# Optimization experiments

Measured on AMD Instinct MI355X. Metric: run time of the kernel, lower is better.

## Reference

```python
import jax, jax.numpy as jnp
import numpy as np

N_HEAD = 16
W = 128  # one-sided window = attention_window // 2


def setup_inputs() -> dict:
    key = jax.random.key(0)
    ks = jax.random.split(key, 6)
    B, S, D = 4, 1536, 1024
    init = lambda k: jax.random.normal(k, (D, D), jnp.float32) * 0.02
    return {
        "x": jax.random.normal(ks[0], (B, S, D), jnp.float32),
        "Wq": init(ks[1]), "bq": jnp.zeros((D,), jnp.float32),
        "Wk": init(ks[2]),
        "Wv": init(ks[3]), "bv": jnp.zeros((D,), jnp.float32),
        "Wo": init(ks[4]), "bo": jnp.zeros((D,), jnp.float32),
    }


def _local_attention(q, k, v, w):
    """Sliding-window attention. q,k,v: [B,H,S,Dh]; q,k pre-scaled.
    Returns context [B,H,S,Dh] and banded logits qk [B,S,H,2w+1] (fp32)."""
    B, H, S, Dh = q.shape
    C = S // w  # number of w-sized query chunks
    pad = [(0, 0), (0, 0), (w, w), (0, 0)]
    kp = jnp.pad(k, pad)
    vp = jnp.pad(v, pad)
    # key/value chunks: chunk c sees padded positions [c*w, c*w + 3w)
    idx = jnp.arange(C)[:, None] * w + jnp.arange(3 * w)[None, :]  # [C,3w]
    kc = kp[:, :, idx]                      # [B,H,C,3w,Dh]
    vc = vp[:, :, idx]                      # [B,H,C,3w,Dh]
    qc = q.reshape(B, H, C, w, Dh)          # [B,H,C,w,Dh]
    scores = jnp.einsum('bhcxd,bhcyd->bhcxy', qc, kc)  # [B,H,C,w,3w]
    # extract diagonal band: query x attends to chunk-local keys y = x .. x+2w
    xi = jnp.arange(w)[:, None]             # [w,1]
    jj = jnp.arange(2 * w + 1)[None, :]     # [1,2w+1]
    y = xi + jj                             # [w,2w+1], values in [0,3w)
    band = jnp.take_along_axis(scores, y[None, None, None], axis=-1)  # [B,H,C,w,2w+1]
    # mask positions whose absolute key index falls outside [0,S)
    key_pos = jnp.arange(C)[:, None, None] * w + xi[None] + jj[None] - w  # [C,w,2w+1]
    valid = (key_pos >= 0) & (key_pos < S)
    band = jnp.where(valid[None, None], band, -jnp.inf)
    prob = jax.nn.softmax(band.astype(jnp.float32), axis=-1).astype(q.dtype)
    # scatter band probs back to chunk layout, then contract with value chunks
    scat = jnp.zeros_like(scores).at[..., xi, y].set(prob)  # [B,H,C,w,3w]
    ctx = jnp.einsum('bhcxy,bhcyd->bhcxd', scat, vc).reshape(B, H, S, Dh)
    qk = band.astype(jnp.float32).reshape(B, H, S, 2 * w + 1).transpose(0, 2, 1, 3)
    return ctx, qk


def reference(x, Wq, bq, Wk, Wv, bv, Wo, bo):
    B, S, D = x.shape
    H, Dh = N_HEAD, D // N_HEAD
    scale = Dh ** (-0.25)
    q = ((x @ Wq.T + bq).reshape(B, S, H, Dh).transpose(0, 2, 1, 3)) * scale
    k = ((x @ Wk.T).reshape(B, S, H, Dh).transpose(0, 2, 1, 3)) * scale
    v = (x @ Wv.T + bv).reshape(B, S, H, Dh).transpose(0, 2, 1, 3)
    ctx, qk = _local_attention(q, k, v, W)
    wv = ctx.transpose(0, 2, 1, 3).reshape(B, S, D)
    out = wv @ Wo.T + bo
    return out, qk
```

## Files before the change

kernel.cpp:

```cpp
#include <hip/hip_runtime.h>

#define S_LEN  1536
#define NH     16
#define DHEAD  64
#define WIN    128
#define BAND   257
#define DMODEL 1024
#define BATCH  4
#define MROWS  (BATCH * S_LEN)

#define SQ    32
#define SWIN  (SQ + 2*WIN)
#define WKEYS 320
#define PST   296

#define NEG_BIG (-3.0e38f)

typedef __attribute__((ext_vector_type(8))) short frag_ab;
typedef __attribute__((ext_vector_type(4))) float frag_cd;
typedef __attribute__((ext_vector_type(8))) unsigned short ushort8v;

__device__ __forceinline__ unsigned short f2bf(float f) {
  unsigned u = __float_as_uint(f);
  u += 0x7FFFu + ((u >> 16) & 1u);
  return (unsigned short)(u >> 16);
}
__device__ __forceinline__ float bf2f(unsigned short h) {
  return __uint_as_float(((unsigned)h) << 16);
}

__device__ __forceinline__ void gload16(const unsigned short* g, unsigned short* l) {
  __builtin_amdgcn_global_load_lds(
      (const __attribute__((address_space(1))) unsigned int*)g,
      (__attribute__((address_space(3))) unsigned int*)l, 16, 0, 0);
}

__device__ __forceinline__ int swz4(int r) { return (r & 3) ^ ((r >> 2) & 3); }

__global__ __launch_bounds__(256)
void convert_hilo(const float* __restrict__ src, unsigned short* __restrict__ hi,
                  unsigned short* __restrict__ lo, int n4)
{
  const int i = blockIdx.x * 256 + threadIdx.x;
  if (i >= n4) return;
  const float4 v = reinterpret_cast<const float4*>(src)[i];
  unsigned short h0 = f2bf(v.x), h1 = f2bf(v.y), h2 = f2bf(v.z), h3 = f2bf(v.w);
  unsigned short l0 = f2bf(v.x - bf2f(h0)), l1 = f2bf(v.y - bf2f(h1));
  unsigned short l2 = f2bf(v.z - bf2f(h2)), l3 = f2bf(v.w - bf2f(h3));
  uint2 hp, lp;
  hp.x = (unsigned)h0 | ((unsigned)h1 << 16); hp.y = (unsigned)h2 | ((unsigned)h3 << 16);
  lp.x = (unsigned)l0 | ((unsigned)l1 << 16); lp.y = (unsigned)l2 | ((unsigned)l3 << 16);
  reinterpret_cast<uint2*>(hi)[i] = hp;
  reinterpret_cast<uint2*>(lo)[i] = lp;
}

__global__ __launch_bounds__(256)
void copy_f4(const float4* __restrict__ src, float4* __restrict__ dst, int n4)
{
  const int i = blockIdx.x * 256 + threadIdx.x;
  if (i < n4) dst[i] = src[i];
}

__global__ __launch_bounds__(256)
void mfma_gemm_qkv(const unsigned short* __restrict__ Ah_g,
                   const unsigned short* __restrict__ Al_g,
                   const unsigned short* __restrict__ Bh_g,
                   const unsigned short* __restrict__ Bl_g,
                   const float* __restrict__ bq, const float* __restrict__ bv,
                   float scale,
                   unsigned short* __restrict__ Qh, unsigned short* __restrict__ Ql,
                   unsigned short* __restrict__ Kh, unsigned short* __restrict__ Kl,
                   unsigned short* __restrict__ Vh, unsigned short* __restrict__ Vl)
{
  __shared__ __align__(16) unsigned short Ah[128*32];
  __shared__ __align__(16) unsigned short Al[128*32];
  __shared__ __align__(16) unsigned short Bh[128*32];
  __shared__ __align__(16) unsigned short Bl[128*32];

  const int t    = threadIdx.x;
  const int wave = t >> 6, lane = t & 63;
  const int wr   = wave >> 1, wc = wave & 1;

  const int bid  = blockIdx.x;
  const int xcd  = bid & 7;
  const int r    = bid >> 3;
  const int n0   = (xcd*3 + (r % 3)) * 128;
  const int m0   = (r / 3) * 128;

  frag_cd acc[4][4];
#pragma unroll
  for (int i = 0; i < 4; ++i)
#pragma unroll
    for (int j = 0; j < 4; ++j) acc[i][j] = (frag_cd){0.f,0.f,0.f,0.f};

  const int srow = lane >> 2;
  const int scol = ((lane & 3) ^ swz4(srow)) * 8;
  const unsigned short* pa0 = Ah_g + (size_t)(m0 + wave*32      + srow) * DMODEL + scol;
  const unsigned short* pa1 = Ah_g + (size_t)(m0 + wave*32 + 16 + srow) * DMODEL + scol;
  const unsigned short* qa0 = Al_g + (size_t)(m0 + wave*32      + srow) * DMODEL + scol;
  const unsigned short* qa1 = Al_g + (size_t)(m0 + wave*32 + 16 + srow) * DMODEL + scol;
  const unsigned short* pb0 = Bh_g + (size_t)(n0 + wave*32      + srow) * DMODEL + scol;
  const unsigned short* pb1 = Bh_g + (size_t)(n0 + wave*32 + 16 + srow) * DMODEL + scol;
  const unsigned short* qb0 = Bl_g + (size_t)(n0 + wave*32      + srow) * DMODEL + scol;
  const unsigned short* qb1 = Bl_g + (size_t)(n0 + wave*32 + 16 + srow) * DMODEL + scol;
  unsigned short* lA0 = &Ah[(wave*32)*32];
  unsigned short* lA1 = &Ah[(wave*32+16)*32];
  unsigned short* lL0 = &Al[(wave*32)*32];
  unsigned short* lL1 = &Al[(wave*32+16)*32];
  unsigned short* lB0 = &Bh[(wave*32)*32];
  unsigned short* lB1 = &Bh[(wave*32+16)*32];
  unsigned short* lC0 = &Bl[(wave*32)*32];
  unsigned short* lC1 = &Bl[(wave*32+16)*32];

  const int l16  = lane & 15;
  const int koff = ((lane >> 4) * 8) ^ (swz4(l16) * 8);
  int ofsA[4], ofsB[4];
#pragma unroll
  for (int i = 0; i < 4; ++i) ofsA[i] = (wr*64 + i*16 + l16)*32 + koff;
#pragma unroll
  for (int j = 0; j < 4; ++j) ofsB[j] = (wc*64 + j*16 + l16)*32 + koff;

  for (int k0 = 0; k0 < DMODEL; k0 += 32) {
    gload16(pa0, lA0); gload16(pa1, lA1);
    gload16(qa0, lL0); gload16(qa1, lL1);
    gload16(pb0, lB0); gload16(pb1, lB1);
    gload16(qb0, lC0); gload16(qb1, lC1);
    pa0 += 32; pa1 += 32; qa0 += 32; qa1 += 32;
    pb0 += 32; pb1 += 32; qb0 += 32; qb1 += 32;
    __syncthreads();

    frag_ab ah[4], alr[4];
#pragma unroll
    for (int i = 0; i < 4; ++i) {
      ah[i]  = *reinterpret_cast<const frag_ab*>(&Ah[ofsA[i]]);
      alr[i] = *reinterpret_cast<const frag_ab*>(&Al[ofsA[i]]);
    }
#pragma unroll
    for (int j = 0; j < 4; ++j) {
      frag_ab bh  = *reinterpret_cast<const frag_ab*>(&Bh[ofsB[j]]);
      frag_ab blr = *reinterpret_cast<const frag_ab*>(&Bl[ofsB[j]]);
#pragma unroll
      for (int i = 0; i < 4; ++i) {
        acc[i][j] = __builtin_amdgcn_mfma_f32_16x16x32_bf16(ah[i],  bh,  acc[i][j], 0,0,0);
        acc[i][j] = __builtin_amdgcn_mfma_f32_16x16x32_bf16(ah[i],  blr, acc[i][j], 0,0,0);
        acc[i][j] = __builtin_amdgcn_mfma_f32_16x16x32_bf16(alr[i], bh,  acc[i][j], 0,0,0);
      }
    }
    __syncthreads();
  }

  const int rg = lane >> 4;
  const int which = n0 >> 10;
  const float sc = (which < 2) ? scale : 1.0f;
  const float* bias = (which == 0) ? bq : ((which == 2) ? bv : nullptr);
  unsigned short* Dh = (which == 0) ? Qh : ((which == 1) ? Kh : Vh);
  unsigned short* Dl = (which == 0) ? Ql : ((which == 1) ? Kl : Vl);
#pragma unroll
  for (int j = 0; j < 4; ++j) {
    const int n  = n0 + wc*64 + j*16 + l16;
    const int nn = n & 1023;
    const float bval = bias ? bias[nn] : 0.f;
    const int hh = nn >> 6, dh = nn & 63;
#pragma unroll
    for (int i = 0; i < 4; ++i) {
#pragma unroll
      for (int r2 = 0; r2 < 4; ++r2) {
        const int m = m0 + wr*64 + i*16 + rg*4 + r2;
        const int b = m / S_LEN;
        const int s = m - b * S_LEN;
        const size_t idx = ((size_t)((b*NH + hh)*S_LEN + s))*DHEAD + dh;
        const float v = (acc[i][j][r2] + bval) * sc;
        const unsigned short hv = f2bf(v);
        Dh[idx] = hv;
        Dl[idx] = f2bf(v - bf2f(hv));
      }
    }
  }
}

__global__ __launch_bounds__(256)
void mfma_gemm_bt(const unsigned short* __restrict__ Ah_g,
                  const unsigned short* __restrict__ Al_g,
                  const unsigned short* __restrict__ Bh_g,
                  const unsigned short* __restrict__ Bl_g,
                  const float* __restrict__ bias, float scale,
                  float* __restrict__ Cf)
{
  __shared__ __align__(16) unsigned short Ah[128*32];
  __shared__ __align__(16) unsigned short Al[128*32];
  __shared__ __align__(16) unsigned short Bh[64*32];
  __shared__ __align__(16) unsigned short Bl[64*32];

  const int t    = threadIdx.x;
  const int wave = t >> 6, lane = t & 63;
  const int wr   = wave >> 1, wc = wave & 1;
  const int m0   = blockIdx.y * 128;
  const int n0   = blockIdx.x * 64;

  frag_cd acc[4][2];
#pragma unroll
  for (int i = 0; i < 4; ++i)
#pragma unroll
    for (int j = 0; j < 2; ++j) acc[i][j] = (frag_cd){0.f,0.f,0.f,0.f};

  const int srow = lane >> 2;
  const int scol = ((lane & 3) ^ swz4(srow)) * 8;
  const unsigned short* pa0 = Ah_g + (size_t)(m0 + wave*32      + srow) * DMODEL + scol;
  const unsigned short* pa1 = Ah_g + (size_t)(m0 + wave*32 + 16 + srow) * DMODEL + scol;
  const unsigned short* qa0 = Al_g + (size_t)(m0 + wave*32      + srow) * DMODEL + scol;
  const unsigned short* qa1 = Al_g + (size_t)(m0 + wave*32 + 16 + srow) * DMODEL + scol;
  const unsigned short* pb  = Bh_g + (size_t)(n0 + wave*16      + srow) * DMODEL + scol;
  const unsigned short* qb  = Bl_g + (size_t)(n0 + wave*16      + srow) * DMODEL + scol;
  unsigned short* lA0 = &Ah[(wave*32)*32];
  unsigned short* lA1 = &Ah[(wave*32+16)*32];
  unsigned short* lL0 = &Al[(wave*32)*32];
  unsigned short* lL1 = &Al[(wave*32+16)*32];
  unsigned short* lB  = &Bh[(wave*16)*32];
  unsigned short* lBl = &Bl[(wave*16)*32];

  const int l16  = lane & 15;
  const int koff = ((lane >> 4) * 8) ^ (swz4(l16) * 8);
  int ofsA[4], ofsB[2];
#pragma unroll
  for (int i = 0; i < 4; ++i) ofsA[i] = (wr*64 + i*16 + l16)*32 + koff;
#pragma unroll
  for (int j = 0; j < 2; ++j) ofsB[j] = (wc*32 + j*16 + l16)*32 + koff;

  for (int k0 = 0; k0 < DMODEL; k0 += 32) {
    gload16(pa0, lA0); gload16(pa1, lA1);
    gload16(qa0, lL0); gload16(qa1, lL1);
    gload16(pb,  lB);  gload16(qb,  lBl);
    pa0 += 32; pa1 += 32; qa0 += 32; qa1 += 32; pb += 32; qb += 32;
    __syncthreads();

    frag_ab ah[4], alr[4], bh[2], blr[2];
#pragma unroll
    for (int i = 0; i < 4; ++i) {
      ah[i]  = *reinterpret_cast<const frag_ab*>(&Ah[ofsA[i]]);
      alr[i] = *reinterpret_cast<const frag_ab*>(&Al[ofsA[i]]);
    }
#pragma unroll
    for (int j = 0; j < 2; ++j) {
      bh[j]  = *reinterpret_cast<const frag_ab*>(&Bh[ofsB[j]]);
      blr[j] = *reinterpret_cast<const frag_ab*>(&Bl[ofsB[j]]);
    }
#pragma unroll
    for (int i = 0; i < 4; ++i)
#pragma unroll
      for (int j = 0; j < 2; ++j) {
        acc[i][j] = __builtin_amdgcn_mfma_f32_16x16x32_bf16(ah[i],  bh[j],  acc[i][j], 0,0,0);
        acc[i][j] = __builtin_amdgcn_mfma_f32_16x16x32_bf16(ah[i],  blr[j], acc[i][j], 0,0,0);
        acc[i][j] = __builtin_amdgcn_mfma_f32_16x16x32_bf16(alr[i], bh[j],  acc[i][j], 0,0,0);
      }
    __syncthreads();
  }

  const int rg = lane >> 4;
#pragma unroll
  for (int j = 0; j < 2; ++j) {
    const int n = n0 + wc*32 + j*16 + l16;
    const float bval = bias ? bias[n] : 0.f;
#pragma unroll
    for (int i = 0; i < 4; ++i) {
#pragma unroll
      for (int r = 0; r < 4; ++r) {
        const int m = m0 + wr*64 + i*16 + rg*4 + r;
        Cf[(size_t)m * DMODEL + n] = (acc[i][j][r] + bval) * scale;
      }
    }
  }
}

__global__ __launch_bounds__(256, 3)
void attn_fused(const unsigned short* __restrict__ Qh_g, const unsigned short* __restrict__ Ql_g,
                const unsigned short* __restrict__ Kh_g, const unsigned short* __restrict__ Kl_g,
                const unsigned short* __restrict__ Vh_g, const unsigned short* __restrict__ Vl_g,
                float* __restrict__ qk,
                unsigned short* __restrict__ ctx_hi, unsigned short* __restrict__ ctx_lo)
{
  __shared__ __align__(16) unsigned char arena[48384];
  unsigned short* Khs = (unsigned short*)(arena);
  unsigned short* Kls = (unsigned short*)(arena + 20480);
  unsigned short* Qhs = (unsigned short*)(arena + 40960);
  unsigned short* Qls = (unsigned short*)(arena + 43008);
  unsigned short* Pth = (unsigned short*)(arena);
  unsigned short* Ptl = (unsigned short*)(arena + 18944);
  float*          red = (float*)(arena + 37888);
  unsigned short* Vs  = (unsigned short*)(arena + 38912);

  const int t    = threadIdx.x;
  const int wave = t >> 6, lane = t & 63;

  const int lid  = blockIdx.x;
  const int xcd  = lid & 7;
  const int idx  = lid >> 3;
  const int qblk = xcd*6 + (idx % 6);
  const int hb   = idx / 6;
  const int h    = hb & 15, b = hb >> 4;
  const int qa0  = qblk * SQ;
  const int ws0  = qa0 - WIN;

  const size_t ho = (size_t)(b*NH + h) * S_LEN * DHEAD;
  const unsigned short* Qh = Qh_g + ho;
  const unsigned short* Ql = Ql_g + ho;
  const unsigned short* Kh = Kh_g + ho;
  const unsigned short* Kl = Kl_g + ho;
  const unsigned short* Vh = Vh_g + ho;
  const unsigned short* Vl = Vl_g + ho;

  const int l16  = lane & 15;
  const int grp  = lane >> 4;
  const int koff  = grp * 8;
  const int koffs = koff ^ (swz4(l16) * 8);
  const int srow = lane >> 2;
  const int scol = ((lane & 3) ^ swz4(srow)) * 8;

  frag_cd acc[2][5];
#pragma unroll
  for (int tm = 0; tm < 2; ++tm)
#pragma unroll
    for (int tn = 0; tn < 5; ++tn) acc[tm][tn] = (frag_cd){0.f,0.f,0.f,0.f};

  for (int p = 0; p < 2; ++p) {
    const int d0 = p * 32;
    if (p) __syncthreads();
#pragma unroll
    for (int i = 0; i < 5; ++i) {
      const int r0 = wave*80 + i*16;
      const ptrdiff_t g = (ptrdiff_t)(ws0 + r0 + srow) * DHEAD + d0 + scol;
      gload16(Kh + g, &Khs[r0*32]);
      gload16(Kl + g, &Kls[r0*32]);
    }
    if (wave < 2) {
      const unsigned short* src = wave ? Ql : Qh;
      unsigned short* dst = wave ? Qls : Qhs;
#pragma unroll
      for (int i = 0; i < 2; ++i) {
        const ptrdiff_t g = (ptrdiff_t)(qa0 + i*16 + srow) * DHEAD + d0 + scol;
        gload16(src + g, &dst[i*16*32]);
      }
    }
    __syncthreads();

    frag_ab ah[2], al[2];
#pragma unroll
    for (int tm = 0; tm < 2; ++tm) {
      const int o = (tm*16 + l16)*32 + koffs;
      ah[tm] = *reinterpret_cast<const frag_ab*>(&Qhs[o]);
      al[tm] = *reinterpret_cast<const frag_ab*>(&Qls[o]);
    }
#pragma unroll
    for (int tn = 0; tn < 5; ++tn) {
      const int o = (wave*80 + tn*16 + l16)*32 + koffs;
      frag_ab bh = *reinterpret_cast<const frag_ab*>(&Khs[o]);
      frag_ab bl = *reinterpret_cast<const frag_ab*>(&Kls[o]);
#pragma unroll
      for (int tm = 0; tm < 2; ++tm) {
        acc[tm][tn] = __builtin_amdgcn_mfma_f32_16x16x32_bf16(ah[tm], bh, acc[tm][tn], 0,0,0);
        acc[tm][tn] = __builtin_amdgcn_mfma_f32_16x16x32_bf16(ah[tm], bl, acc[tm][tn], 0,0,0);
        acc[tm][tn] = __builtin_amdgcn_mfma_f32_16x16x32_bf16(al[tm], bh, acc[tm][tn], 0,0,0);
      }
    }
  }

#pragma unroll
  for (int tm = 0; tm < 2; ++tm)
#pragma unroll
    for (int tn = 0; tn < 5; ++tn)
#pragma unroll
      for (int r = 0; r < 4; ++r) {
        const int x  = tm*16 + grp*4 + r;
        const int yw = wave*80 + tn*16 + l16;
        const int j  = yw - x;
        const int kp = ws0 + yw;
        const bool ok = (j >= 0) & (j < BAND) & (kp >= 0) & (kp < S_LEN);
        acc[tm][tn][r] = ok ? acc[tm][tn][r] : NEG_BIG;
      }
#pragma unroll
  for (int tm = 0; tm < 2; ++tm)
#pragma unroll
    for (int r = 0; r < 4; ++r) {
      const int x = tm*16 + grp*4 + r;
      float* qrow = qk + ((size_t)(b*S_LEN + qa0 + x)*NH + h) * BAND;
#pragma unroll
      for (int tn = 0; tn < 5; ++tn) {
        const int yw = wave*80 + tn*16 + l16;
        const int j  = yw - x;
        if (j >= 0 && j < BAND) qrow[j] = acc[tm][tn][r];
      }
    }

  __syncthreads();

  const unsigned short* vsrc = (wave == 3) ? Vl : Vh;
  const int vrow0 = (wave == 3) ? 8 : 0;
  ushort8v RA[5], RB[5];

  auto loadVto = [&](int c, ushort8v* R) {
    const int d0 = c*8;
#pragma unroll
    for (int it = 0; it < 5; ++it) {
      const int y = it*64 + lane;
      ushort8v v = {0,0,0,0,0,0,0,0};
      if (y < SWIN) {
        const int kp = ws0 + y;
        if (kp >= 0 && kp < S_LEN)
          v = *reinterpret_cast<const ushort8v*>(vsrc + (size_t)kp*DHEAD + d0);
      }
      R[it] = v;
    }
  };
  auto writeVfrom = [&](ushort8v* R) {
#pragma unroll
    for (int it = 0; it < 5; ++it) {
      const int y = it*64 + lane;
      if (y < SWIN) {
#pragma unroll
        for (int e = 0; e < 8; ++e) Vs[(vrow0 + e)*PST + y] = R[it][e];
      }
    }
  };

  if (wave >= 2) loadVto(0, RA);
#pragma unroll
  for (int tm = 0; tm < 2; ++tm)
#pragma unroll
    for (int r = 0; r < 4; ++r) {
      float m = acc[tm][0][r];
#pragma unroll
      for (int tn = 1; tn < 5; ++tn) m = fmaxf(m, acc[tm][tn][r]);
      m = fmaxf(m, __shfl_xor(m, 1, 64));
      m = fmaxf(m, __shfl_xor(m, 2, 64));
      m = fmaxf(m, __shfl_xor(m, 4, 64));
      m = fmaxf(m, __shfl_xor(m, 8, 64));
      if (l16 == 0) red[(0*4 + wave)*32 + tm*16 + grp*4 + r] = m;
    }
  {
    const uint4 z = make_uint4(0u,0u,0u,0u);
    uint4* pz = reinterpret_cast<uint4*>(arena);
    for (int i = t; i < 37888/16; i += 256) pz[i] = z;
  }
  if (wave >= 2) writeVfrom(RA);
  __syncthreads();

  if (wave >= 2) loadVto(1, RA);
#pragma unroll
  for (int tm = 0; tm < 2; ++tm)
#pragma unroll
    for (int r = 0; r < 4; ++r) {
      const int x = tm*16 + grp*4 + r;
      float m = red[0*128 + 0*32 + x];
      m = fmaxf(m, red[0*128 + 1*32 + x]);
      m = fmaxf(m, red[0*128 + 2*32 + x]);
      m = fmaxf(m, red[0*128 + 3*32 + x]);
      float s = 0.f;
#pragma unroll
      for (int tn = 0; tn < 5; ++tn) {
        const float e = __expf(acc[tm][tn][r] - m);
        acc[tm][tn][r] = e;
        s += e;
      }
      s += __shfl_xor(s, 1, 64);
      s += __shfl_xor(s, 2, 64);
      s += __shfl_xor(s, 4, 64);
      s += __shfl_xor(s, 8, 64);
      if (l16 == 0) red[(1*4 + wave)*32 + x] = s;
    }
  __syncthreads();

#pragma unroll
  for (int tm = 0; tm < 2; ++tm)
#pragma unroll
    for (int r = 0; r < 4; ++r) {
      const int x = tm*16 + grp*4 + r;
      const float gs = red[128 + 0*32 + x] + red[128 + 1*32 + x]
                     + red[128 + 2*32 + x] + red[128 + 3*32 + x];
      const float inv = 1.f / gs;
#pragma unroll
      for (int tn = 0; tn < 5; ++tn) {
        const int yw = wave*80 + tn*16 + l16;
        const int j  = yw - x;
        if (yw < SWIN && j >= 0 && j < BAND) {
          const float p = acc[tm][tn][r] * inv;
          const unsigned short ph = f2bf(p);
          Pth[x*PST + yw] = ph;
          Ptl[x*PST + yw] = f2bf(p - bf2f(ph));
        }
      }
    }
  __syncthreads();

  frag_ab phf[9];
  if (wave < 2) {
#pragma unroll
    for (int ks = 0; ks < 9; ++ks)
      phf[ks] = *reinterpret_cast<const frag_ab*>(&Pth[(wave*16 + l16)*PST + ks*32 + koff]);
  }

#pragma unroll
  for (int c = 0; c < 8; ++c) {
    frag_cd pacc = (frag_cd){0.f,0.f,0.f,0.f};
    if (wave < 2) {
#pragma unroll
      for (int ks = 0; ks < 9; ++ks) {
        const int kk = ks*32 + koff;
        frag_ab pl = *reinterpret_cast<const frag_ab*>(&Ptl[(wave*16 + l16)*PST + kk]);
        frag_ab vb = *reinterpret_cast<const frag_ab*>(&Vs[l16*PST + kk]);
        pacc = __builtin_amdgcn_mfma_f32_16x16x32_bf16(phf[ks], vb, pacc, 0,0,0);
        pacc = __builtin_amdgcn_mfma_f32_16x16x32_bf16(pl,      vb, pacc, 0,0,0);
      }
    } else {
      if (c < 6) loadVto(c + 2, (c & 1) ? RA : RB);
    }
    __syncthreads();
    if (wave < 2) {
#pragma unroll
      for (int r = 0; r < 4; ++r) pacc[r] += __shfl_xor(pacc[r], 8, 64);
      if (l16 < 8) {
        const int d = c*8 + l16;
#pragma unroll
        for (int r = 0; r < 4; ++r) {
          const int x = wave*16 + grp*4 + r;
          const size_t oidx = ((size_t)(b*S_LEN + qa0 + x))*DMODEL + h*DHEAD + d;
          const float v = pacc[r];
          const unsigned short hv = f2bf(v);
          ctx_hi[oidx] = hv;
          ctx_lo[oidx] = f2bf(v - bf2f(hv));
        }
      }
    } else {
      if (c < 7) writeVfrom((c & 1) ? RB : RA);
    }
    if (c < 7) __syncthreads();
  }
}

extern "C" void kernel_launch(void* const* d_in, const int* in_sizes, int n_in,
                              void* d_out, int out_size, void* d_ws, size_t ws_size,
                              hipStream_t stream) {
  const float* x  = (const float*)d_in[0];
  const float* Wq = (const float*)d_in[1];
  const float* bq = (const float*)d_in[2];
  const float* Wk = (const float*)d_in[3];
  const float* Wv = (const float*)d_in[4];
  const float* bv = (const float*)d_in[5];
  const float* Wo = (const float*)d_in[6];
  const float* bo = (const float*)d_in[7];

  float* out = (float*)d_out;
  float* qk  = out + (size_t)MROWS * DMODEL;

  const size_t NX = (size_t)MROWS * DMODEL;
  const size_t NW = (size_t)DMODEL * DMODEL;

  unsigned short* xh  = (unsigned short*)qk;
  unsigned short* xl  = xh  + NX;
  unsigned short* whc = xl  + NX;
  unsigned short* wlc = whc + 3*NW;

  unsigned short* Qh = (unsigned short*)d_ws;
  unsigned short* Ql = Qh + NX;
  unsigned short* Kh = Ql + NX;
  unsigned short* Kl = Kh + NX;
  unsigned short* Vh = Kl + NX;
  unsigned short* Vl = Vh + NX;

  unsigned short* ctxh = (unsigned short*)out;
  unsigned short* ctxl = ctxh + NX;
  unsigned short* woh  = Kh;
  unsigned short* wol  = Kh + NW;
  float* outTmp = (float*)d_ws;

  const float scale = 0.35355339059327373f;

  dim3 blk(256);
  hipLaunchKernelGGL(convert_hilo, dim3(NX/1024), blk, 0, stream, x,  xh,  xl,  (int)(NX/4));
  hipLaunchKernelGGL(convert_hilo, dim3(NW/1024), blk, 0, stream, Wq, whc,        wlc,        (int)(NW/4));
  hipLaunchKernelGGL(convert_hilo, dim3(NW/1024), blk, 0, stream, Wk, whc + NW,   wlc + NW,   (int)(NW/4));
  hipLaunchKernelGGL(convert_hilo, dim3(NW/1024), blk, 0, stream, Wv, whc + 2*NW, wlc + 2*NW, (int)(NW/4));

  hipLaunchKernelGGL(mfma_gemm_qkv, dim3(1152), blk, 0, stream,
                     xh, xl, whc, wlc, bq, bv, scale,
                     Qh, Ql, Kh, Kl, Vh, Vl);

  hipLaunchKernelGGL(attn_fused, dim3((S_LEN/SQ)*NH*BATCH), blk, 0, stream,
                     Qh, Ql, Kh, Kl, Vh, Vl, qk, ctxh, ctxl);

  hipLaunchKernelGGL(convert_hilo, dim3(NW/1024), blk, 0, stream, Wo, woh, wol, (int)(NW/4));

  dim3 gg(DMODEL/64, MROWS/128);
  hipLaunchKernelGGL(mfma_gemm_bt, gg, blk, 0, stream, ctxh, ctxl, woh, wol, bo, 1.0f,
                     outTmp);
  hipLaunchKernelGGL(copy_f4, dim3(NX/1024), blk, 0, stream,
                     (const float4*)outTmp, (float4*)out, (int)(NX/4));
}
```

Before: 483.2 us.

## Write Wo GEMM output directly, store head-major ctx, enlarge QKV tiles

The output projection GEMM now writes straight into the final output buffer, which removes the temporary buffer and the separate copy kernel. The attention context is now stored in head-major layout, reusing the Q workspace, and the Wo GEMM gathers its A operand from that layout. The QKV GEMM tile grows from 128x128 to 256x128, which halves the grid and doubles the accumulators per wave. The larger tile raises register and LDS use and may reduce occupancy. The Wo GEMM's A-operand loads become strided per head instead of contiguous rows.

```diff
diff --git a/kernel.cpp b/kernel.cpp
--- a/kernel.cpp
+++ b/kernel.cpp
@@ -55,13 +55,6 @@
 }
 
 __global__ __launch_bounds__(256)
-void copy_f4(const float4* __restrict__ src, float4* __restrict__ dst, int n4)
-{
-  const int i = blockIdx.x * 256 + threadIdx.x;
-  if (i < n4) dst[i] = src[i];
-}
-
-__global__ __launch_bounds__(256)
 void mfma_gemm_qkv(const unsigned short* __restrict__ Ah_g,
                    const unsigned short* __restrict__ Al_g,
                    const unsigned short* __restrict__ Bh_g,
@@ -72,8 +65,8 @@
                    unsigned short* __restrict__ Kh, unsigned short* __restrict__ Kl,
                    unsigned short* __restrict__ Vh, unsigned short* __restrict__ Vl)
 {
-  __shared__ __align__(16) unsigned short Ah[128*32];
-  __shared__ __align__(16) unsigned short Al[128*32];
+  __shared__ __align__(16) unsigned short Ah[256*32];
+  __shared__ __align__(16) unsigned short Al[256*32];
   __shared__ __align__(16) unsigned short Bh[128*32];
   __shared__ __align__(16) unsigned short Bl[128*32];
 
@@ -85,65 +78,61 @@
   const int xcd  = bid & 7;
   const int r    = bid >> 3;
   const int n0   = (xcd*3 + (r % 3)) * 128;
-  const int m0   = (r / 3) * 128;
-
-  frag_cd acc[4][4];
-#pragma unroll
-  for (int i = 0; i < 4; ++i)
+  const int m0   = (r / 3) * 256;
+
+  frag_cd acc[8][4];
+#pragma unroll
+  for (int i = 0; i < 8; ++i)
 #pragma unroll
     for (int j = 0; j < 4; ++j) acc[i][j] = (frag_cd){0.f,0.f,0.f,0.f};
 
   const int srow = lane >> 2;
   const int scol = ((lane & 3) ^ swz4(srow)) * 8;
-  const unsigned short* pa0 = Ah_g + (size_t)(m0 + wave*32      + srow) * DMODEL + scol;
-  const unsigned short* pa1 = Ah_g + (size_t)(m0 + wave*32 + 16 + srow) * DMODEL + scol;
-  const unsigned short* qa0 = Al_g + (size_t)(m0 + wave*32      + srow) * DMODEL + scol;
-  const unsigned short* qa1 = Al_g + (size_t)(m0 + wave*32 + 16 + srow) * DMODEL + scol;
-  const unsigned short* pb0 = Bh_g + (size_t)(n0 + wave*32      + srow) * DMODEL + scol;
-  const unsigned short* pb1 = Bh_g + (size_t)(n0 + wave*32 + 16 + srow) * DMODEL + scol;
-  const unsigned short* qb0 = Bl_g + (size_t)(n0 + wave*32      + srow) * DMODEL + scol;
-  const unsigned short* qb1 = Bl_g + (size_t)(n0 + wave*32 + 16 + srow) * DMODEL + scol;
-  unsigned short* lA0 = &Ah[(wave*32)*32];
-  unsigned short* lA1 = &Ah[(wave*32+16)*32];
-  unsigned short* lL0 = &Al[(wave*32)*32];
-  unsigned short* lL1 = &Al[(wave*32+16)*32];
-  unsigned short* lB0 = &Bh[(wave*32)*32];
-  unsigned short* lB1 = &Bh[(wave*32+16)*32];
-  unsigned short* lC0 = &Bl[(wave*32)*32];
-  unsigned short* lC1 = &Bl[(wave*32+16)*32];
+  const unsigned short* aSh = Ah_g + (size_t)(m0 + wave*64 + srow) * DMODEL + scol;
+  const unsigned short* aSl = Al_g + (size_t)(m0 + wave*64 + srow) * DMODEL + scol;
+  const unsigned short* bSh = Bh_g + (size_t)(n0 + wave*32 + srow) * DMODEL + scol;
+  const unsigned short* bSl = Bl_g + (size_t)(n0 + wave*32 + srow) * DMODEL + scol;
+  unsigned short* aDh = &Ah[(wave*64)*32];
+  unsigned short* aDl = &Al[(wave*64)*32];
+  unsigned short* bDh = &Bh[(wave*32)*32];
+  unsigned short* bDl = &Bl[(wave*32)*32];
 
   const int l16  = lane & 15;
   const int koff = ((lane >> 4) * 8) ^ (swz4(l16) * 8);
-  int ofsA[4], ofsB[4];
-#pragma unroll
-  for (int i = 0; i < 4; ++i) ofsA[i] = (wr*64 + i*16 + l16)*32 + koff;
+  int ofsA[8], ofsB[4];
+#pragma unroll
+  for (int i = 0; i < 8; ++i) ofsA[i] = (wr*128 + i*16 + l16)*32 + koff;
 #pragma unroll
   for (int j = 0; j < 4; ++j) ofsB[j] = (wc*64 + j*16 + l16)*32 + koff;
 
   for (int k0 = 0; k0 < DMODEL; k0 += 32) {
-    gload16(pa0, lA0); gload16(pa1, lA1);
-    gload16(qa0, lL0); gload16(qa1, lL1);
-    gload16(pb0, lB0); gload16(pb1, lB1);
-    gload16(qb0, lC0); gload16(qb1, lC1);
-    pa0 += 32; pa1 += 32; qa0 += 32; qa1 += 32;
-    pb0 += 32; pb1 += 32; qb0 += 32; qb1 += 32;
+#pragma unroll
+    for (int u = 0; u < 4; ++u) {
+      gload16(aSh + (size_t)u*16*DMODEL + k0, aDh + u*16*32);
+      gload16(aSl + (size_t)u*16*DMODEL + k0, aDl + u*16*32);
+    }
+#pragma unroll
+    for (int u = 0; u < 2; ++u) {
+      gload16(bSh + (size_t)u*16*DMODEL + k0, bDh + u*16*32);
+      gload16(bSl + (size_t)u*16*DMODEL + k0, bDl + u*16*32);
+    }
     __syncthreads();
 
-    frag_ab ah[4], alr[4];
-#pragma unroll
-    for (int i = 0; i < 4; ++i) {
-      ah[i]  = *reinterpret_cast<const frag_ab*>(&Ah[ofsA[i]]);
-      alr[i] = *reinterpret_cast<const frag_ab*>(&Al[ofsA[i]]);
-    }
+    frag_ab bh[4], blr[4];
 #pragma unroll
     for (int j = 0; j < 4; ++j) {
-      frag_ab bh  = *reinterpret_cast<const frag_ab*>(&Bh[ofsB[j]]);
-      frag_ab blr = *reinterpret_cast<const frag_ab*>(&Bl[ofsB[j]]);
-#pragma unroll
-      for (int i = 0; i < 4; ++i) {
-        acc[i][j] = __builtin_amdgcn_mfma_f32_16x16x32_bf16(ah[i],  bh,  acc[i][j], 0,0,0);
-        acc[i][j] = __builtin_amdgcn_mfma_f32_16x16x32_bf16(ah[i],  blr, acc[i][j], 0,0,0);
-        acc[i][j] = __builtin_amdgcn_mfma_f32_16x16x32_bf16(alr[i], bh,  acc[i][j], 0,0,0);
+      bh[j]  = *reinterpret_cast<const frag_ab*>(&Bh[ofsB[j]]);
+      blr[j] = *reinterpret_cast<const frag_ab*>(&Bl[ofsB[j]]);
+    }
+#pragma unroll
+    for (int i = 0; i < 8; ++i) {
+      frag_ab ah  = *reinterpret_cast<const frag_ab*>(&Ah[ofsA[i]]);
+      frag_ab alr = *reinterpret_cast<const frag_ab*>(&Al[ofsA[i]]);
+#pragma unroll
+      for (int j = 0; j < 4; ++j) {
+        acc[i][j] = __builtin_amdgcn_mfma_f32_16x16x32_bf16(ah,  bh[j],  acc[i][j], 0,0,0);
+        acc[i][j] = __builtin_amdgcn_mfma_f32_16x16x32_bf16(ah,  blr[j], acc[i][j], 0,0,0);
+        acc[i][j] = __builtin_amdgcn_mfma_f32_16x16x32_bf16(alr, bh[j],  acc[i][j], 0,0,0);
       }
     }
     __syncthreads();
@@ -162,10 +151,10 @@
     const float bval = bias ? bias[nn] : 0.f;
     const int hh = nn >> 6, dh = nn & 63;
 #pragma unroll
-    for (int i = 0; i < 4; ++i) {
+    for (int i = 0; i < 8; ++i) {
 #pragma unroll
       for (int r2 = 0; r2 < 4; ++r2) {
-        const int m = m0 + wr*64 + i*16 + rg*4 + r2;
+        const int m = m0 + wr*128 + i*16 + rg*4 + r2;
         const int b = m / S_LEN;
         const int s = m - b * S_LEN;
         const size_t idx = ((size_t)((b*NH + hh)*S_LEN + s))*DHEAD + dh;
@@ -179,11 +168,11 @@
 }
 
 __global__ __launch_bounds__(256)
-void mfma_gemm_bt(const unsigned short* __restrict__ Ah_g,
+void mfma_gemm_wo(const unsigned short* __restrict__ Ah_g,
                   const unsigned short* __restrict__ Al_g,
                   const unsigned short* __restrict__ Bh_g,
                   const unsigned short* __restrict__ Bl_g,
-                  const float* __restrict__ bias, float scale,
+                  const float* __restrict__ bias,
                   float* __restrict__ Cf)
 {
   __shared__ __align__(16) unsigned short Ah[128*32];
@@ -205,12 +194,16 @@
 
   const int srow = lane >> 2;
   const int scol = ((lane & 3) ^ swz4(srow)) * 8;
-  const unsigned short* pa0 = Ah_g + (size_t)(m0 + wave*32      + srow) * DMODEL + scol;
-  const unsigned short* pa1 = Ah_g + (size_t)(m0 + wave*32 + 16 + srow) * DMODEL + scol;
-  const unsigned short* qa0 = Al_g + (size_t)(m0 + wave*32      + srow) * DMODEL + scol;
-  const unsigned short* qa1 = Al_g + (size_t)(m0 + wave*32 + 16 + srow) * DMODEL + scol;
-  const unsigned short* pb  = Bh_g + (size_t)(n0 + wave*16      + srow) * DMODEL + scol;
-  const unsigned short* qb  = Bl_g + (size_t)(n0 + wave*16      + srow) * DMODEL + scol;
+  size_t rbase[2];
+#pragma unroll
+  for (int u = 0; u < 2; ++u) {
+    const int m = m0 + wave*32 + u*16 + srow;
+    const int b = m / S_LEN;
+    const int s = m - b * S_LEN;
+    rbase[u] = ((size_t)(b*NH))*S_LEN*DHEAD + (size_t)s*DHEAD;
+  }
+  const unsigned short* pb = Bh_g + (size_t)(n0 + wave*16 + srow) * DMODEL + scol;
+  const unsigned short* qb = Bl_g + (size_t)(n0 + wave*16 + srow) * DMODEL + scol;
   unsigned short* lA0 = &Ah[(wave*32)*32];
   unsigned short* lA1 = &Ah[(wave*32+16)*32];
   unsigned short* lL0 = &Al[(wave*32)*32];
@@ -227,10 +220,14 @@
   for (int j = 0; j < 2; ++j) ofsB[j] = (wc*32 + j*16 + l16)*32 + koff;
 
   for (int k0 = 0; k0 < DMODEL; k0 += 32) {
-    gload16(pa0, lA0); gload16(pa1, lA1);
-    gload16(qa0, lL0); gload16(qa1, lL1);
-    gload16(pb,  lB);  gload16(qb,  lBl);
-    pa0 += 32; pa1 += 32; qa0 += 32; qa1 += 32; pb += 32; qb += 32;
+    const int kk = k0 + scol;
+    const size_t aoff = ((size_t)(kk >> 6))*(S_LEN*DHEAD) + (kk & 63);
+    gload16(Ah_g + rbase[0] + aoff, lA0);
+    gload16(Ah_g + rbase[1] + aoff, lA1);
+    gload16(Al_g + rbase[0] + aoff, lL0);
+    gload16(Al_g + rbase[1] + aoff, lL1);
+    gload16(pb, lB);  gload16(qb, lBl);
+    pb += 32; qb += 32;
     __syncthreads();
 
     frag_ab ah[4], alr[4], bh[2], blr[2];
@@ -259,13 +256,13 @@
 #pragma unroll
   for (int j = 0; j < 2; ++j) {
     const int n = n0 + wc*32 + j*16 + l16;
-    const float bval = bias ? bias[n] : 0.f;
+    const float bval = bias[n];
 #pragma unroll
     for (int i = 0; i < 4; ++i) {
 #pragma unroll
       for (int r = 0; r < 4; ++r) {
         const int m = m0 + wr*64 + i*16 + rg*4 + r;
-        Cf[(size_t)m * DMODEL + n] = (acc[i][j][r] + bval) * scale;
+        Cf[(size_t)m * DMODEL + n] = acc[i][j][r] + bval;
       }
     }
   }
@@ -521,7 +518,7 @@
 #pragma unroll
         for (int r = 0; r < 4; ++r) {
           const int x = wave*16 + grp*4 + r;
-          const size_t oidx = ((size_t)(b*S_LEN + qa0 + x))*DMODEL + h*DHEAD + d;
+          const size_t oidx = ho + (size_t)(qa0 + x)*DHEAD + d;
           const float v = pacc[r];
           const unsigned short hv = f2bf(v);
           ctx_hi[oidx] = hv;
@@ -565,11 +562,10 @@
   unsigned short* Vh = Kl + NX;
   unsigned short* Vl = Vh + NX;
 
-  unsigned short* ctxh = (unsigned short*)out;
-  unsigned short* ctxl = ctxh + NX;
+  unsigned short* ctxh = Qh;
+  unsigned short* ctxl = Ql;
   unsigned short* woh  = Kh;
   unsigned short* wol  = Kh + NW;
-  float* outTmp = (float*)d_ws;
 
   const float scale = 0.35355339059327373f;
 
@@ -579,7 +575,7 @@
   hipLaunchKernelGGL(convert_hilo, dim3(NW/1024), blk, 0, stream, Wk, whc + NW,   wlc + NW,   (int)(NW/4));
   hipLaunchKernelGGL(convert_hilo, dim3(NW/1024), blk, 0, stream, Wv, whc + 2*NW, wlc + 2*NW, (int)(NW/4));
 
-  hipLaunchKernelGGL(mfma_gemm_qkv, dim3(1152), blk, 0, stream,
+  hipLaunchKernelGGL(mfma_gemm_qkv, dim3(576), blk, 0, stream,
                      xh, xl, whc, wlc, bq, bv, scale,
                      Qh, Ql, Kh, Kl, Vh, Vl);
 
@@ -589,8 +585,5 @@
   hipLaunchKernelGGL(convert_hilo, dim3(NW/1024), blk, 0, stream, Wo, woh, wol, (int)(NW/4));
 
   dim3 gg(DMODEL/64, MROWS/128);
-  hipLaunchKernelGGL(mfma_gemm_bt, gg, blk, 0, stream, ctxh, ctxl, woh, wol, bo, 1.0f,
-                     outTmp);
-  hipLaunchKernelGGL(copy_f4, dim3(NX/1024), blk, 0, stream,
-                     (const float4*)outTmp, (float4*)out, (int)(NX/4));
-}
+  hipLaunchKernelGGL(mfma_gemm_wo, gg, blk, 0, stream, ctxh, ctxl, woh, wol, bo, out);
+}
```

Measured after the change: 550.1 us. 1.14x slower.
